# Kernel tuning notes

Measured on AMD Instinct MI355X. Metric: run time of the kernel, lower is better.

Reference implementation:

```python
import jax, jax.numpy as jnp
import numpy as np

N_NODES = 100000

def graph_conv(x, edge_index, w_root, w_rel, b):
    # PyG GraphConv (aggr='add'): out = aggr(x_j) @ W_rel + b + x @ W_root
    src, dst = edge_index[0], edge_index[1]
    msgs = x[src]                                   # [E, F_in] gather
    agg = jax.ops.segment_sum(msgs, dst, num_segments=N_NODES)  # [N, F_in] scatter-add
    return agg @ w_rel + b + x @ w_root             # [N, F_out]


def setup_inputs() -> dict:
    key = jax.random.key(0)
    ks = jax.random.split(key, 12)
    E = 1600000
    return {
        "x": jax.random.normal(ks[0], (N_NODES, 16), dtype=jnp.float32),
        "edge_index": jax.random.randint(ks[1], (2, E), 0, N_NODES, dtype=jnp.int64),
        "w_root1": jax.random.normal(ks[2], (16, 32), dtype=jnp.float32) * 0.1,
        "w_rel1": jax.random.normal(ks[3], (16, 32), dtype=jnp.float32) * 0.1,
        "b1": jax.random.normal(ks[4], (32,), dtype=jnp.float32) * 0.1,
        "w_root2": jax.random.normal(ks[5], (32, 64), dtype=jnp.float32) * 0.1,
        "w_rel2": jax.random.normal(ks[6], (32, 64), dtype=jnp.float32) * 0.1,
        "b2": jax.random.normal(ks[7], (64,), dtype=jnp.float32) * 0.1,
        "fc1_w": jax.random.normal(ks[8], (64, 32), dtype=jnp.float32) * 0.1,
        "fc1_b": jax.random.normal(ks[9], (32,), dtype=jnp.float32) * 0.1,
        "fc2_w": jax.random.normal(ks[10], (32, 16), dtype=jnp.float32) * 0.1,
        "fc2_b": jax.random.normal(ks[11], (16,), dtype=jnp.float32) * 0.1,
    }


def reference(x, edge_index, w_root1, w_rel1, b1, w_root2, w_rel2, b2,
              fc1_w, fc1_b, fc2_w, fc2_b):
    h = jax.nn.relu(graph_conv(x, edge_index, w_root1, w_rel1, b1))   # [N, 32]
    h = jax.nn.relu(graph_conv(h, edge_index, w_root2, w_rel2, b2))   # [N, 64]
    h = jax.nn.relu(h @ fc1_w + fc1_b)                                 # [N, 32]
    return h @ fc2_w + fc2_b                                           # [N, 16]
```

## Files before the change

### kernel.cpp

```cpp
#include <hip/hip_runtime.h>

#define F4E(v,i) ((i)==0?(v).x:((i)==1?(v).y:((i)==2?(v).z:(v).w)))

#define CHUNK 4096
#define ITERS 8

__device__ inline float4 shfl4b(float4 v, int src) {
    float4 r;
    r.x = __shfl(v.x, src, 4); r.y = __shfl(v.y, src, 4);
    r.z = __shfl(v.z, src, 4); r.w = __shfl(v.w, src, 4);
    return r;
}
__device__ inline float4 shfl8b(float4 v, int src) {
    float4 r;
    r.x = __shfl(v.x, src, 8); r.y = __shfl(v.y, src, 8);
    r.z = __shfl(v.z, src, 8); r.w = __shfl(v.w, src, 8);
    return r;
}

__device__ inline unsigned packbf2(float a, float b) {
    unsigned ua = __float_as_uint(a), ub = __float_as_uint(b);
    ua = (ua + 0x7fffu + ((ua >> 16) & 1u)) >> 16;
    ub = (ub + 0x7fffu + ((ub >> 16) & 1u)) >> 16;
    return ua | (ub << 16);
}
__device__ inline float bflo(unsigned w) { return __uint_as_float(w << 16); }
__device__ inline float bfhi(unsigned w) { return __uint_as_float(w & 0xffff0000u); }

__global__ __launch_bounds__(256) void k_xcvt(
    const float* __restrict__ x, unsigned short* __restrict__ xb, int n8)
{
    int i = blockIdx.x * 256 + threadIdx.x;
    if (i >= n8) return;
    const float4* xp = reinterpret_cast<const float4*>(x) + (size_t)i * 2;
    float4 a = xp[0], b = xp[1];
    uint4 w;
    w.x = packbf2(a.x, a.y); w.y = packbf2(a.z, a.w);
    w.z = packbf2(b.x, b.y); w.w = packbf2(b.z, b.w);
    reinterpret_cast<uint4*>(xb)[i] = w;
}

__global__ __launch_bounds__(512) void k_bhist(
    const int* __restrict__ ei, int* __restrict__ bhist, int E, int NB)
{
    __shared__ int cnt[512];
    int t = threadIdx.x;
    cnt[t] = 0;
    __syncthreads();
    int base = blockIdx.x * CHUNK;
#pragma unroll
    for (int i = 0; i < ITERS; ++i) {
        int e = base + i * 512 + t;
        if (e < E) {
            int dst = ei[E + e];
            atomicAdd(&cnt[dst >> 8], 1);
        }
    }
    __syncthreads();
    if (t < NB && cnt[t]) atomicAdd(&bhist[t], cnt[t]);
}

__global__ __launch_bounds__(512) void k_bscan(
    const int* __restrict__ bhist, int* __restrict__ bstart,
    int* __restrict__ gcursor, int NB, int E)
{
    __shared__ int s[512];
    int t = threadIdx.x;
    int v0 = (t < NB) ? bhist[t] : 0;
    s[t] = v0;
    __syncthreads();
    for (int off = 1; off < 512; off <<= 1) {
        int v = (t >= off) ? s[t - off] : 0;
        __syncthreads();
        s[t] += v;
        __syncthreads();
    }
    if (t < NB) { int ex = s[t] - v0; bstart[t] = ex; gcursor[t] = ex; }
    if (t == 0) bstart[NB] = E;
}

__global__ __launch_bounds__(512) void k_partition(
    const int* __restrict__ ei, int* __restrict__ gcursor,
    int* __restrict__ epack, int E)
{
    __shared__ int cnt[512], sc[512], lbase[512], gbase[512], lcnt[512];
    __shared__ int stage[CHUNK];
    __shared__ unsigned short stageb[CHUNK];
    int t = threadIdx.x;
    cnt[t] = 0; lcnt[t] = 0;
    __syncthreads();

    int base = blockIdx.x * CHUNK;
    int pk[ITERS], bb[ITERS];
#pragma unroll
    for (int i = 0; i < ITERS; ++i) {
        int e = base + i * 512 + t;
        if (e < E) {
            int src = ei[e], dst = ei[E + e];
            pk[i] = (src << 8) | (dst & 255);
            bb[i] = dst >> 8;
            atomicAdd(&cnt[bb[i]], 1);
        } else bb[i] = -1;
    }
    __syncthreads();

    int v0 = cnt[t];
    sc[t] = v0;
    __syncthreads();
    for (int off = 1; off < 512; off <<= 1) {
        int v = (t >= off) ? sc[t - off] : 0;
        __syncthreads();
        sc[t] += v;
        __syncthreads();
    }
    lbase[t] = sc[t] - v0;
    if (v0 > 0) gbase[t] = atomicAdd(&gcursor[t], v0);
    __syncthreads();

#pragma unroll
    for (int i = 0; i < ITERS; ++i) {
        if (bb[i] >= 0) {
            int loc = atomicAdd(&lcnt[bb[i]], 1);
            int slot = lbase[bb[i]] + loc;
            stage[slot] = pk[i];
            stageb[slot] = (unsigned short)bb[i];
        }
    }
    __syncthreads();

    int m = min(CHUNK, E - base);
#pragma unroll
    for (int i = 0; i < ITERS; ++i) {
        int slot = i * 512 + t;
        if (slot < m) {
            int b = stageb[slot];
            epack[gbase[b] + (slot - lbase[b])] = stage[slot];
        }
    }
}

__global__ __launch_bounds__(256) void k_sort(
    const int* __restrict__ bstart, const int* __restrict__ epack,
    int* __restrict__ rs, int* __restrict__ esorted, int N, int E)
{
    __shared__ int hist[256], cur[256], sc[256];
    int t = threadIdx.x;
    int b = blockIdx.x;
    int s0 = bstart[b], s1 = bstart[b + 1];
    hist[t] = 0;
    __syncthreads();
    for (int e = s0 + t; e < s1; e += 256)
        atomicAdd(&hist[epack[e] & 255], 1);
    __syncthreads();

    int v0 = hist[t];
    sc[t] = v0;
    __syncthreads();
    for (int off = 1; off < 256; off <<= 1) {
        int v = (t >= off) ? sc[t - off] : 0;
        __syncthreads();
        sc[t] += v;
        __syncthreads();
    }
    int excl = sc[t] - v0;
    cur[t] = excl;
    int node = (b << 8) + t;
    if (node < N) rs[node] = s0 + excl;
    if (b == 0 && t == 0) rs[N] = E;
    __syncthreads();

    for (int e = s0 + t; e < s1; e += 256) {
        int pk = epack[e];
        int dlo = pk & 255;
        int pos = s0 + atomicAdd(&cur[dlo], 1);
        esorted[pos] = ((unsigned)pk) >> 8;
    }
}

__global__ __launch_bounds__(256) void k_g1f(
    const float* __restrict__ x, const unsigned short* __restrict__ xb,
    const int* __restrict__ rs, const int* __restrict__ esrc,
    const float* __restrict__ wroot, const float* __restrict__ wrel,
    const float* __restrict__ bias, unsigned short* __restrict__ h1, int N)
{
    __shared__ float4 s_wr[128], s_wl[128], s_b[8];
    int t = threadIdx.x;
    if (t < 128) {
        s_wr[t] = reinterpret_cast<const float4*>(wroot)[t];
        s_wl[t] = reinterpret_cast<const float4*>(wrel)[t];
    }
    if (t < 8) s_b[t] = reinterpret_cast<const float4*>(bias)[t];
    __syncthreads();

    int tid = blockIdx.x * 256 + t;
    int n = tid >> 2, p = tid & 3;
    if (n >= N) return;
    int s0 = rs[n], s1 = rs[n + 1];
    float4 g = make_float4(0.f, 0.f, 0.f, 0.f);
    int e = s0;
    for (; e + 7 < s1; e += 8) {
        uint2 w[8];
#pragma unroll
        for (int u = 0; u < 8; ++u) {
            int src = esrc[e + u];
            w[u] = reinterpret_cast<const uint2*>(xb + (size_t)src * 16)[p];
        }
#pragma unroll
        for (int u = 0; u < 8; ++u) {
            g.x += bflo(w[u].x); g.y += bfhi(w[u].x);
            g.z += bflo(w[u].y); g.w += bfhi(w[u].y);
        }
    }
    for (; e < s1; ++e) {
        int src = esrc[e];
        uint2 w0 = reinterpret_cast<const uint2*>(xb + (size_t)src * 16)[p];
        g.x += bflo(w0.x); g.y += bfhi(w0.x);
        g.z += bflo(w0.y); g.w += bfhi(w0.y);
    }
    float4 a = *reinterpret_cast<const float4*>(x + (size_t)n * 16 + p * 4);

    int jb = p * 2;
    float4 acc0 = s_b[jb], acc1 = s_b[jb + 1];
#pragma unroll
    for (int kc = 0; kc < 4; ++kc) {
        float4 a4 = shfl4b(a, kc);
        float4 g4 = shfl4b(g, kc);
#pragma unroll
        for (int kk = 0; kk < 4; ++kk) {
            float av = F4E(a4, kk), gv = F4E(g4, kk);
            int k = kc * 4 + kk;
            float4 wr0 = s_wr[k * 8 + jb], wr1 = s_wr[k * 8 + jb + 1];
            float4 wl0 = s_wl[k * 8 + jb], wl1 = s_wl[k * 8 + jb + 1];
            acc0.x += av * wr0.x + gv * wl0.x;
            acc0.y += av * wr0.y + gv * wl0.y;
            acc0.z += av * wr0.z + gv * wl0.z;
            acc0.w += av * wr0.w + gv * wl0.w;
            acc1.x += av * wr1.x + gv * wl1.x;
            acc1.y += av * wr1.y + gv * wl1.y;
            acc1.z += av * wr1.z + gv * wl1.z;
            acc1.w += av * wr1.w + gv * wl1.w;
        }
    }
    acc0.x = fmaxf(acc0.x, 0.f); acc0.y = fmaxf(acc0.y, 0.f);
    acc0.z = fmaxf(acc0.z, 0.f); acc0.w = fmaxf(acc0.w, 0.f);
    acc1.x = fmaxf(acc1.x, 0.f); acc1.y = fmaxf(acc1.y, 0.f);
    acc1.z = fmaxf(acc1.z, 0.f); acc1.w = fmaxf(acc1.w, 0.f);

    uint4 w;
    w.x = packbf2(acc0.x, acc0.y);
    w.y = packbf2(acc0.z, acc0.w);
    w.z = packbf2(acc1.x, acc1.y);
    w.w = packbf2(acc1.z, acc1.w);
    reinterpret_cast<uint4*>(h1 + (size_t)n * 32)[p] = w;
}

__global__ __launch_bounds__(256) void k_g2f(
    const unsigned short* __restrict__ h1, const int* __restrict__ rs,
    const int* __restrict__ esrc,
    const float* __restrict__ wroot, const float* __restrict__ wrel,
    const float* __restrict__ bias,
    const float* __restrict__ f1w, const float* __restrict__ f1b,
    const float* __restrict__ f2w, const float* __restrict__ f2b,
    float* __restrict__ out, int N)
{
    __shared__ float4 s_wr[512], s_wl[512], s_b[16];
    __shared__ float4 s_f1[512];
    __shared__ unsigned s_f2u[256];
    __shared__ float4 s_b1[8];
    __shared__ float  s_b2[16];
    int t = threadIdx.x;
    for (int i = t; i < 512; i += 256) {
        s_wr[i] = reinterpret_cast<const float4*>(wroot)[i];
        s_wl[i] = reinterpret_cast<const float4*>(wrel)[i];
        int k = i >> 3, jc = i & 7;
        s_f1[(i & ~7) | ((jc + (k >> 3)) & 7)] = reinterpret_cast<const float4*>(f1w)[i];
    }
    {
        int k2 = t >> 3, jp = t & 7;
        s_f2u[t] = packbf2(f2w[k2 * 16 + jp * 2], f2w[k2 * 16 + jp * 2 + 1]);
    }
    if (t < 16) s_b[t]  = reinterpret_cast<const float4*>(bias)[t];
    if (t < 8)  s_b1[t] = reinterpret_cast<const float4*>(f1b)[t];
    if (t < 16) s_b2[t] = f2b[t];
    __syncthreads();

    int tid = blockIdx.x * 256 + t;
    int n = tid >> 3, p = tid & 7;
    if (n >= N) return;

    int s0 = rs[n], s1 = rs[n + 1];
    float4 g = make_float4(0.f, 0.f, 0.f, 0.f);
    int e = s0;
    for (; e + 7 < s1; e += 8) {
        uint2 w[8];
#pragma unroll
        for (int u = 0; u < 8; ++u) {
            int src = esrc[e + u];
            w[u] = reinterpret_cast<const uint2*>(h1 + (size_t)src * 32)[p];
        }
#pragma unroll
        for (int u = 0; u < 8; ++u) {
            g.x += bflo(w[u].x); g.y += bfhi(w[u].x);
            g.z += bflo(w[u].y); g.w += bfhi(w[u].y);
        }
    }
    for (; e < s1; ++e) {
        int src = esrc[e];
        uint2 w0 = reinterpret_cast<const uint2*>(h1 + (size_t)src * 32)[p];
        g.x += bflo(w0.x); g.y += bfhi(w0.x);
        g.z += bflo(w0.y); g.w += bfhi(w0.y);
    }
    uint2 aw = reinterpret_cast<const uint2*>(h1 + (size_t)n * 32)[p];
    float4 a = make_float4(bflo(aw.x), bfhi(aw.x), bflo(aw.y), bfhi(aw.y));

    int jb = p * 2;
    float4 acc0 = s_b[jb], acc1 = s_b[jb + 1];
#pragma unroll
    for (int kc = 0; kc < 8; ++kc) {
        float4 a4 = shfl8b(a, kc);
        float4 g4 = shfl8b(g, kc);
#pragma unroll
        for (int kk = 0; kk < 4; ++kk) {
            float av = F4E(a4, kk), gv = F4E(g4, kk);
            int k = kc * 4 + kk;
            float4 wr0 = s_wr[k * 16 + jb], wr1 = s_wr[k * 16 + jb + 1];
            float4 wl0 = s_wl[k * 16 + jb], wl1 = s_wl[k * 16 + jb + 1];
            acc0.x += av * wr0.x + gv * wl0.x;
            acc0.y += av * wr0.y + gv * wl0.y;
            acc0.z += av * wr0.z + gv * wl0.z;
            acc0.w += av * wr0.w + gv * wl0.w;
            acc1.x += av * wr1.x + gv * wl1.x;
            acc1.y += av * wr1.y + gv * wl1.y;
            acc1.z += av * wr1.z + gv * wl1.z;
            acc1.w += av * wr1.w + gv * wl1.w;
        }
    }
    acc0.x = fmaxf(acc0.x, 0.f); acc0.y = fmaxf(acc0.y, 0.f);
    acc0.z = fmaxf(acc0.z, 0.f); acc0.w = fmaxf(acc0.w, 0.f);
    acc1.x = fmaxf(acc1.x, 0.f); acc1.y = fmaxf(acc1.y, 0.f);
    acc1.z = fmaxf(acc1.z, 0.f); acc1.w = fmaxf(acc1.w, 0.f);

    float4 f[8];
    float4 z4 = make_float4(0.f, 0.f, 0.f, 0.f);
#pragma unroll
    for (int jc = 0; jc < 8; ++jc) f[jc] = p ? z4 : s_b1[jc];
#pragma unroll
    for (int kk = 0; kk < 8; ++kk) {
        float hv = (kk < 4) ? F4E(acc0, kk) : F4E(acc1, kk - 4);
        int k = p * 8 + kk;
        int row = k * 8;
#pragma unroll
        for (int jc = 0; jc < 8; ++jc) {
            float4 w = s_f1[row | ((jc + p) & 7)];
            f[jc].x += hv * w.x; f[jc].y += hv * w.y;
            f[jc].z += hv * w.z; f[jc].w += hv * w.w;
        }
    }
#pragma unroll
    for (int m = 1; m < 8; m <<= 1) {
#pragma unroll
        for (int jc = 0; jc < 8; ++jc) {
            f[jc].x += __shfl_xor(f[jc].x, m);
            f[jc].y += __shfl_xor(f[jc].y, m);
            f[jc].z += __shfl_xor(f[jc].z, m);
            f[jc].w += __shfl_xor(f[jc].w, m);
        }
    }
#pragma unroll
    for (int jc = 0; jc < 8; ++jc) {
        f[jc].x = fmaxf(f[jc].x, 0.f); f[jc].y = fmaxf(f[jc].y, 0.f);
        f[jc].z = fmaxf(f[jc].z, 0.f); f[jc].w = fmaxf(f[jc].w, 0.f);
    }

    float o0 = s_b2[p * 2], o1 = s_b2[p * 2 + 1];
#pragma unroll
    for (int k2 = 0; k2 < 32; ++k2) {
        float av = F4E(f[k2 >> 2], k2 & 3);
        unsigned wp = s_f2u[k2 * 8 + p];
        o0 += av * bflo(wp);
        o1 += av * bfhi(wp);
    }
    float2* o = reinterpret_cast<float2*>(out + (size_t)n * 16 + p * 2);
    *o = make_float2(o0, o1);
}

extern "C" void kernel_launch(void* const* d_in, const int* in_sizes, int n_in,
                              void* d_out, int out_size, void* d_ws, size_t ws_size,
                              hipStream_t stream)
{
    const float* x   = (const float*)d_in[0];
    const int*   ei  = (const int*)d_in[1];
    const float* wr1 = (const float*)d_in[2];
    const float* wl1 = (const float*)d_in[3];
    const float* b1  = (const float*)d_in[4];
    const float* wr2 = (const float*)d_in[5];
    const float* wl2 = (const float*)d_in[6];
    const float* b2  = (const float*)d_in[7];
    const float* f1w = (const float*)d_in[8];
    const float* f1b = (const float*)d_in[9];
    const float* f2w = (const float*)d_in[10];
    const float* f2b = (const float*)d_in[11];
    float* out = (float*)d_out;

    const int N  = in_sizes[0] / 16;
    const int E  = in_sizes[1] / 2;
    const int NB = (N + 255) >> 8;

    float*          ws      = (float*)d_ws;
    unsigned short* h1      = (unsigned short*)ws;
    unsigned short* xb      = (unsigned short*)(ws + (size_t)N * 16);
    int*            esorted = (int*)(ws + (size_t)N * 24);
    int*            epack   = esorted + E;
    int*            rs      = epack + E;
    int*            bhist   = rs + N + 1;
    int*            bstart  = bhist + NB;
    int*            gcursor = bstart + NB + 1;

    hipMemsetAsync(bhist, 0, (size_t)NB * sizeof(int), stream);

    int nchunk = (E + CHUNK - 1) / CHUNK;
    int g_cv = (N * 2 + 255) / 256;
    int g_g1 = (N * 4 + 255) / 256;
    int g_g2 = (N * 8 + 255) / 256;

    k_xcvt     <<<g_cv,   256, 0, stream>>>(x, xb, N * 2);
    k_bhist    <<<nchunk, 512, 0, stream>>>(ei, bhist, E, NB);
    k_bscan    <<<1,      512, 0, stream>>>(bhist, bstart, gcursor, NB, E);
    k_partition<<<nchunk, 512, 0, stream>>>(ei, gcursor, epack, E);
    k_sort     <<<NB,     256, 0, stream>>>(bstart, epack, rs, esorted, N, E);

    k_g1f      <<<g_g1, 256, 0, stream>>>(x, xb, rs, esorted, wr1, wl1, b1, h1, N);
    k_g2f      <<<g_g2, 256, 0, stream>>>(h1, rs, esorted, wr2, wl2, b2,
                                          f1w, f1b, f2w, f2b, out, N);
}
```

Before: 215.9 us.

## Use bf16 MFMA for layer-2 and MLP matmuls in fused gather kernel

Rewrites the second graph-conv kernel so that each wavefront handles a 16-node tile. The root, relation and two fully connected matmuls now run as 16x16x32 bf16 MFMA instructions with register-resident bf16 weight fragments, in place of scalar FMAs over shared-memory weights and shuffles. The gather now uses 4 lanes per node with 16-byte loads instead of 8 lanes with 8-byte loads. Intermediate activations pass through per-wave LDS tiles, and aggregated features and activations are rounded to bf16, which adds precision loss. Each thread also re-reads and converts all weights from global memory, and the block-wide shared weight staging and its barrier are removed.

```diff
diff --git a/kernel.cpp b/kernel.cpp
--- a/kernel.cpp
+++ b/kernel.cpp
@@ -4,6 +4,9 @@
 
 #define CHUNK 4096
 #define ITERS 8
+
+typedef __attribute__((ext_vector_type(8))) short short8;
+typedef __attribute__((ext_vector_type(4))) float f32x4;
 
 __device__ inline float4 shfl4b(float4 v, int src) {
     float4 r;
@@ -11,18 +14,16 @@
     r.z = __shfl(v.z, src, 4); r.w = __shfl(v.w, src, 4);
     return r;
 }
-__device__ inline float4 shfl8b(float4 v, int src) {
-    float4 r;
-    r.x = __shfl(v.x, src, 8); r.y = __shfl(v.y, src, 8);
-    r.z = __shfl(v.z, src, 8); r.w = __shfl(v.w, src, 8);
-    return r;
-}
 
 __device__ inline unsigned packbf2(float a, float b) {
     unsigned ua = __float_as_uint(a), ub = __float_as_uint(b);
     ua = (ua + 0x7fffu + ((ua >> 16) & 1u)) >> 16;
     ub = (ub + 0x7fffu + ((ub >> 16) & 1u)) >> 16;
     return ua | (ub << 16);
+}
+__device__ inline unsigned short bf16r(float f) {
+    unsigned u = __float_as_uint(f);
+    return (unsigned short)((u + 0x7fffu + ((u >> 16) & 1u)) >> 16);
 }
 __device__ inline float bflo(unsigned w) { return __uint_as_float(w << 16); }
 __device__ inline float bfhi(unsigned w) { return __uint_as_float(w & 0xffff0000u); }
@@ -263,125 +264,124 @@
     const float* __restrict__ f2w, const float* __restrict__ f2b,
     float* __restrict__ out, int N)
 {
-    __shared__ float4 s_wr[512], s_wl[512], s_b[16];
-    __shared__ float4 s_f1[512];
-    __shared__ unsigned s_f2u[256];
-    __shared__ float4 s_b1[8];
-    __shared__ float  s_b2[16];
-    int t = threadIdx.x;
-    for (int i = t; i < 512; i += 256) {
-        s_wr[i] = reinterpret_cast<const float4*>(wroot)[i];
-        s_wl[i] = reinterpret_cast<const float4*>(wrel)[i];
-        int k = i >> 3, jc = i & 7;
-        s_f1[(i & ~7) | ((jc + (k >> 3)) & 7)] = reinterpret_cast<const float4*>(f1w)[i];
-    }
+    __shared__ __attribute__((aligned(16))) unsigned short h2l[4][16][72];
+    __shared__ __attribute__((aligned(16))) unsigned short fl[4][16][40];
+
+    int t = threadIdx.x;
+    int w = t >> 6, l = t & 63;
+    int m = l & 15, q4 = l >> 4;
+    int tile = blockIdx.x * 4 + w;
+    int nb = tile * 16;
+    if (nb >= N) return;
+
+    short8 fwr[4], fwl[4];
+#pragma unroll
+    for (int nt = 0; nt < 4; ++nt) {
+#pragma unroll
+        for (int i = 0; i < 8; ++i) {
+            int k = q4 * 8 + i, j = nt * 16 + m;
+            fwr[nt][i] = (short)bf16r(wroot[k * 64 + j]);
+            fwl[nt][i] = (short)bf16r(wrel[k * 64 + j]);
+        }
+    }
+    short8 ff1[2][2];
+#pragma unroll
+    for (int ks = 0; ks < 2; ++ks)
+#pragma unroll
+        for (int nt = 0; nt < 2; ++nt)
+#pragma unroll
+            for (int i = 0; i < 8; ++i)
+                ff1[ks][nt][i] = (short)bf16r(f1w[(ks * 32 + q4 * 8 + i) * 32 + nt * 16 + m]);
+    short8 ff2;
+#pragma unroll
+    for (int i = 0; i < 8; ++i)
+        ff2[i] = (short)bf16r(f2w[(q4 * 8 + i) * 16 + m]);
+
+    int n = nb + m;
+    int s0 = 0, s1 = 0;
+    if (n < N) { s0 = rs[n]; s1 = rs[n + 1]; }
+    float ga0 = 0, ga1 = 0, ga2 = 0, ga3 = 0, ga4 = 0, ga5 = 0, ga6 = 0, ga7 = 0;
+#define ACC8(W) { ga0 += bflo((W).x); ga1 += bfhi((W).x); \
+                  ga2 += bflo((W).y); ga3 += bfhi((W).y); \
+                  ga4 += bflo((W).z); ga5 += bfhi((W).z); \
+                  ga6 += bflo((W).w); ga7 += bfhi((W).w); }
+    int e = s0;
+    for (; e + 3 < s1; e += 4) {
+        int sa = esrc[e], sb = esrc[e + 1], sc2 = esrc[e + 2], sd = esrc[e + 3];
+        uint4 wa = *reinterpret_cast<const uint4*>(h1 + (size_t)sa * 32 + q4 * 8);
+        uint4 wb = *reinterpret_cast<const uint4*>(h1 + (size_t)sb * 32 + q4 * 8);
+        uint4 wc = *reinterpret_cast<const uint4*>(h1 + (size_t)sc2 * 32 + q4 * 8);
+        uint4 wd = *reinterpret_cast<const uint4*>(h1 + (size_t)sd * 32 + q4 * 8);
+        ACC8(wa) ACC8(wb) ACC8(wc) ACC8(wd)
+    }
+    for (; e < s1; ++e) {
+        int sa = esrc[e];
+        uint4 wa = *reinterpret_cast<const uint4*>(h1 + (size_t)sa * 32 + q4 * 8);
+        ACC8(wa)
+    }
+#undef ACC8
+
+    short8 af;
     {
-        int k2 = t >> 3, jp = t & 7;
-        s_f2u[t] = packbf2(f2w[k2 * 16 + jp * 2], f2w[k2 * 16 + jp * 2 + 1]);
-    }
-    if (t < 16) s_b[t]  = reinterpret_cast<const float4*>(bias)[t];
-    if (t < 8)  s_b1[t] = reinterpret_cast<const float4*>(f1b)[t];
-    if (t < 16) s_b2[t] = f2b[t];
-    __syncthreads();
-
-    int tid = blockIdx.x * 256 + t;
-    int n = tid >> 3, p = tid & 7;
-    if (n >= N) return;
-
-    int s0 = rs[n], s1 = rs[n + 1];
-    float4 g = make_float4(0.f, 0.f, 0.f, 0.f);
-    int e = s0;
-    for (; e + 7 < s1; e += 8) {
-        uint2 w[8];
-#pragma unroll
-        for (int u = 0; u < 8; ++u) {
-            int src = esrc[e + u];
-            w[u] = reinterpret_cast<const uint2*>(h1 + (size_t)src * 32)[p];
-        }
-#pragma unroll
-        for (int u = 0; u < 8; ++u) {
-            g.x += bflo(w[u].x); g.y += bfhi(w[u].x);
-            g.z += bflo(w[u].y); g.w += bfhi(w[u].y);
-        }
-    }
-    for (; e < s1; ++e) {
-        int src = esrc[e];
-        uint2 w0 = reinterpret_cast<const uint2*>(h1 + (size_t)src * 32)[p];
-        g.x += bflo(w0.x); g.y += bfhi(w0.x);
-        g.z += bflo(w0.y); g.w += bfhi(w0.y);
-    }
-    uint2 aw = reinterpret_cast<const uint2*>(h1 + (size_t)n * 32)[p];
-    float4 a = make_float4(bflo(aw.x), bfhi(aw.x), bflo(aw.y), bfhi(aw.y));
-
-    int jb = p * 2;
-    float4 acc0 = s_b[jb], acc1 = s_b[jb + 1];
-#pragma unroll
-    for (int kc = 0; kc < 8; ++kc) {
-        float4 a4 = shfl8b(a, kc);
-        float4 g4 = shfl8b(g, kc);
-#pragma unroll
-        for (int kk = 0; kk < 4; ++kk) {
-            float av = F4E(a4, kk), gv = F4E(g4, kk);
-            int k = kc * 4 + kk;
-            float4 wr0 = s_wr[k * 16 + jb], wr1 = s_wr[k * 16 + jb + 1];
-            float4 wl0 = s_wl[k * 16 + jb], wl1 = s_wl[k * 16 + jb + 1];
-            acc0.x += av * wr0.x + gv * wl0.x;
-            acc0.y += av * wr0.y + gv * wl0.y;
-            acc0.z += av * wr0.z + gv * wl0.z;
-            acc0.w += av * wr0.w + gv * wl0.w;
-            acc1.x += av * wr1.x + gv * wl1.x;
-            acc1.y += av * wr1.y + gv * wl1.y;
-            acc1.z += av * wr1.z + gv * wl1.z;
-            acc1.w += av * wr1.w + gv * wl1.w;
-        }
-    }
-    acc0.x = fmaxf(acc0.x, 0.f); acc0.y = fmaxf(acc0.y, 0.f);
-    acc0.z = fmaxf(acc0.z, 0.f); acc0.w = fmaxf(acc0.w, 0.f);
-    acc1.x = fmaxf(acc1.x, 0.f); acc1.y = fmaxf(acc1.y, 0.f);
-    acc1.z = fmaxf(acc1.z, 0.f); acc1.w = fmaxf(acc1.w, 0.f);
-
-    float4 f[8];
-    float4 z4 = make_float4(0.f, 0.f, 0.f, 0.f);
-#pragma unroll
-    for (int jc = 0; jc < 8; ++jc) f[jc] = p ? z4 : s_b1[jc];
-#pragma unroll
-    for (int kk = 0; kk < 8; ++kk) {
-        float hv = (kk < 4) ? F4E(acc0, kk) : F4E(acc1, kk - 4);
-        int k = p * 8 + kk;
-        int row = k * 8;
-#pragma unroll
-        for (int jc = 0; jc < 8; ++jc) {
-            float4 w = s_f1[row | ((jc + p) & 7)];
-            f[jc].x += hv * w.x; f[jc].y += hv * w.y;
-            f[jc].z += hv * w.z; f[jc].w += hv * w.w;
-        }
-    }
-#pragma unroll
-    for (int m = 1; m < 8; m <<= 1) {
-#pragma unroll
-        for (int jc = 0; jc < 8; ++jc) {
-            f[jc].x += __shfl_xor(f[jc].x, m);
-            f[jc].y += __shfl_xor(f[jc].y, m);
-            f[jc].z += __shfl_xor(f[jc].z, m);
-            f[jc].w += __shfl_xor(f[jc].w, m);
-        }
-    }
-#pragma unroll
-    for (int jc = 0; jc < 8; ++jc) {
-        f[jc].x = fmaxf(f[jc].x, 0.f); f[jc].y = fmaxf(f[jc].y, 0.f);
-        f[jc].z = fmaxf(f[jc].z, 0.f); f[jc].w = fmaxf(f[jc].w, 0.f);
-    }
-
-    float o0 = s_b2[p * 2], o1 = s_b2[p * 2 + 1];
-#pragma unroll
-    for (int k2 = 0; k2 < 32; ++k2) {
-        float av = F4E(f[k2 >> 2], k2 & 3);
-        unsigned wp = s_f2u[k2 * 8 + p];
-        o0 += av * bflo(wp);
-        o1 += av * bfhi(wp);
-    }
-    float2* o = reinterpret_cast<float2*>(out + (size_t)n * 16 + p * 2);
-    *o = make_float2(o0, o1);
+        uint4 av = make_uint4(0, 0, 0, 0);
+        if (n < N) av = *reinterpret_cast<const uint4*>(h1 + (size_t)n * 32 + q4 * 8);
+        __builtin_memcpy(&af, &av, 16);
+    }
+    short8 gf;
+    gf[0] = (short)bf16r(ga0); gf[1] = (short)bf16r(ga1);
+    gf[2] = (short)bf16r(ga2); gf[3] = (short)bf16r(ga3);
+    gf[4] = (short)bf16r(ga4); gf[5] = (short)bf16r(ga5);
+    gf[6] = (short)bf16r(ga6); gf[7] = (short)bf16r(ga7);
+
+    f32x4 acc[4];
+#pragma unroll
+    for (int nt = 0; nt < 4; ++nt) {
+        float bj = bias[nt * 16 + m];
+        acc[nt] = (f32x4){bj, bj, bj, bj};
+        acc[nt] = __builtin_amdgcn_mfma_f32_16x16x32_bf16(af, fwr[nt], acc[nt], 0, 0, 0);
+        acc[nt] = __builtin_amdgcn_mfma_f32_16x16x32_bf16(gf, fwl[nt], acc[nt], 0, 0, 0);
+    }
+#pragma unroll
+    for (int nt = 0; nt < 4; ++nt)
+#pragma unroll
+        for (int r = 0; r < 4; ++r)
+            h2l[w][q4 * 4 + r][nt * 16 + m] = bf16r(fmaxf(acc[nt][r], 0.f));
+
+    short8 h2a[2];
+#pragma unroll
+    for (int ks = 0; ks < 2; ++ks) {
+        uint4 v = *reinterpret_cast<const uint4*>(&h2l[w][m][ks * 32 + q4 * 8]);
+        __builtin_memcpy(&h2a[ks], &v, 16);
+    }
+
+    f32x4 fa[2];
+#pragma unroll
+    for (int nt = 0; nt < 2; ++nt) {
+        float bj = f1b[nt * 16 + m];
+        fa[nt] = (f32x4){bj, bj, bj, bj};
+        fa[nt] = __builtin_amdgcn_mfma_f32_16x16x32_bf16(h2a[0], ff1[0][nt], fa[nt], 0, 0, 0);
+        fa[nt] = __builtin_amdgcn_mfma_f32_16x16x32_bf16(h2a[1], ff1[1][nt], fa[nt], 0, 0, 0);
+    }
+#pragma unroll
+    for (int nt = 0; nt < 2; ++nt)
+#pragma unroll
+        for (int r = 0; r < 4; ++r)
+            fl[w][q4 * 4 + r][nt * 16 + m] = bf16r(fmaxf(fa[nt][r], 0.f));
+
+    short8 ffr;
+    {
+        uint4 v = *reinterpret_cast<const uint4*>(&fl[w][m][q4 * 8]);
+        __builtin_memcpy(&ffr, &v, 16);
+    }
+
+    float bj2 = f2b[m];
+    f32x4 oacc = (f32x4){bj2, bj2, bj2, bj2};
+    oacc = __builtin_amdgcn_mfma_f32_16x16x32_bf16(ffr, ff2, oacc, 0, 0, 0);
+#pragma unroll
+    for (int r = 0; r < 4; ++r) {
+        int node = nb + q4 * 4 + r;
+        if (node < N) out[(size_t)node * 16 + m] = oacc[r];
+    }
 }
 
 extern "C" void kernel_launch(void* const* d_in, const int* in_sizes, int n_in,
@@ -421,7 +421,7 @@
     int nchunk = (E + CHUNK - 1) / CHUNK;
     int g_cv = (N * 2 + 255) / 256;
     int g_g1 = (N * 4 + 255) / 256;
-    int g_g2 = (N * 8 + 255) / 256;
+    int g_g2 = (N + 63) / 64;
 
     k_xcvt     <<<g_cv,   256, 0, stream>>>(x, xb, N * 2);
     k_bhist    <<<nchunk, 512, 0, stream>>>(ei, bhist, E, NB);
```

New measurement: 197.7 us. -8.4%, faster.
